# Kernel optimization log

Measured on AMD Instinct MI355X. Metric: run time of the kernel, lower is better.

The kernel has to match this reference:

```python
import jax, jax.numpy as jnp
import numpy as np
from jax import lax

N, T, K = 20000, 512, 12  # K = num_factors + 4


def setup_inputs() -> dict:
    key = jax.random.key(0)
    k1, k2, k3 = jax.random.split(key, 3)
    y = jax.random.normal(k1, (N, T), dtype=jnp.float32)
    f = jax.random.normal(k2, (T, K - 4), dtype=jnp.float32)
    # GARCH params must satisfy omega>0, a+b<1 for stationarity; scale uniforms
    theta = jax.random.uniform(k3, (N, T + 1, K), dtype=jnp.float32) * 0.4 + 0.01
    return {"y": y, "f": f, "theta": theta}


def reference(y, f, theta):
    th = theta[:, 1:, :]                      # [N, T, K]
    a = th[:, :, -3]                          # [N, T]
    b = th[:, :, -2]
    omega = th[:, :, -1]
    a_plus_b = a + b
    # epsilon = y - intercept - sum_f loadings * factors
    eps = y - th[:, :, 0] - jnp.einsum('ntf,tf->nt', th[:, :, 1:-3], f)
    eps2 = jnp.square(eps)
    # unconditional-variance init
    sigma2_0 = omega[:, 0] + a_plus_b[:, 0] * (
        jnp.mean(omega, axis=1) / (1.0 - jnp.mean(a_plus_b, axis=1)))
    # recurrence sigma2[t] = omega[t] + a[t]*sigma2[t-1] + b[t]*eps2[t-1]
    xs = (omega[:, 1:].T, a[:, 1:].T, b[:, 1:].T, eps2[:, :-1].T)  # time-major [T-1, N]

    def step(s, x):
        o_t, a_t, b_t, e_t = x
        s_new = o_t + a_t * s + b_t * e_t
        return s_new, s_new

    _, rest = lax.scan(step, sigma2_0, xs)    # rest: [T-1, N]
    sigma2 = jnp.concatenate([sigma2_0[:, None], rest.T], axis=1)  # [N, T]
    loss = jnp.mean(eps2 / sigma2 + jnp.log(sigma2))
    return (loss, eps, sigma2)
```

## Files before the change

### kernel.cpp

```cpp
#include <hip/hip_runtime.h>

#define N_ROWS 20000
#define T_DIM  512
#define K_DIM  12
#define TH_ROW ((T_DIM + 1) * K_DIM)
#define NBLK   (N_ROWS / 4)

__device__ __forceinline__ float fast_rcp(float x) { return __builtin_amdgcn_rcpf(x); }

__device__ __forceinline__ int tads(int tl) { return 9 * (tl >> 3) + (tl & 7); }

__device__ __forceinline__ void scan_chunk(
    const float* __restrict__ la, const float* __restrict__ lb,
    const float* __restrict__ lo, const float* __restrict__ le,
    int lane, int c, float s0, float& s_carry, float& e2_carry,
    float* __restrict__ sig_row, float& lsum)
{
    const int base = 9 * (lane >> 1) + 4 * (lane & 1);
    float av[4], bv[4], ov[4], e2v[4];
    #pragma unroll
    for (int i = 0; i < 4; ++i) {
        av[i] = la[base + i]; bv[i] = lb[base + i];
        ov[i] = lo[base + i]; e2v[i] = le[base + i];
    }
    float ep0 = e2_carry;
    if (lane > 0) ep0 = le[tads(4 * lane - 1)];

    float cv[4];
    cv[0] = fmaf(bv[0], ep0,    ov[0]);
    cv[1] = fmaf(bv[1], e2v[0], ov[1]);
    cv[2] = fmaf(bv[2], e2v[1], ov[2]);
    cv[3] = fmaf(bv[3], e2v[2], ov[3]);
    if (c == 0 && lane == 0) { av[0] = 0.f; cv[0] = s0; }

    float A = av[0], B = cv[0];
    #pragma unroll
    for (int i = 1; i < 4; ++i) { B = fmaf(av[i], B, cv[i]); A = av[i] * A; }

    float sA = A, sB = B;
    #pragma unroll
    for (int d = 1; d < 64; d <<= 1) {
        float Ap = __shfl_up(sA, d);
        float Bp = __shfl_up(sB, d);
        if (lane >= d) { sB = fmaf(sA, Bp, sB); sA = sA * Ap; }
    }
    float exA = __shfl_up(sA, 1), exB = __shfl_up(sB, 1);
    if (lane == 0) { exA = 1.f; exB = 0.f; }
    float s = fmaf(exA, s_carry, exB);

    #pragma unroll
    for (int i = 0; i < 4; ++i) {
        s = fmaf(av[i], s, cv[i]);
        sig_row[c * 256 + 4 * lane + i] = s;
        lsum += e2v[i] * fast_rcp(s) + __logf(s);
    }
    s_carry  = __shfl(s, 63);
    e2_carry = __shfl(e2v[3], 63);
}

__global__ __launch_bounds__(256) void garch_kernel(
    const float* __restrict__ y,
    const float* __restrict__ f,
    const float* __restrict__ theta,
    float* __restrict__ ws_part,
    float* __restrict__ out_eps,
    float* __restrict__ out_sig)
{
    __shared__ float lds_f[T_DIM * 9];
    __shared__ float lds_scan[4][4 * 288];
    __shared__ float lds_part[4];

    const int tid = threadIdx.x;
    for (int idx = tid; idx < T_DIM * 8; idx += 256) {
        int t = idx >> 3, j = idx & 7;
        lds_f[t * 9 + j] = f[idx];
    }
    __syncthreads();

    const int wave = tid >> 6;
    const int lane = tid & 63;
    const int n = blockIdx.x * 4 + wave;

    float* const wb = &lds_scan[wave][0];
    float* const la = wb;
    float* const lb = wb + 288;
    float* const lo = wb + 576;
    float* const le = wb + 864;

    const float* th_row = theta + (size_t)n * TH_ROW;
    const float* y_row  = y + (size_t)n * T_DIM;
    float* eps_row = out_eps + (size_t)n * T_DIM;
    float* sig_row = out_sig + (size_t)n * T_DIM;

    float a1[4], b1[4], o1[4], e1[4];
    float osum = 0.f, absum = 0.f;

    float4 pv0[4], pv1[4], pv2[4];
    float  py[4];
    #pragma unroll
    for (int i = 0; i < 4; ++i) {
        const int t = i * 64 + lane;
        const float4* p = (const float4*)(th_row + (size_t)(t + 1) * K_DIM);
        pv0[i] = p[0]; pv1[i] = p[1]; pv2[i] = p[2];
        py[i]  = y_row[t];
    }
    __builtin_amdgcn_sched_barrier(0);

    #pragma unroll
    for (int i = 0; i < 8; ++i) {
        const int slot = i & 3;
        const int t = i * 64 + lane;
        const float4 v0 = pv0[slot], v1 = pv1[slot], v2 = pv2[slot];
        const float  yv = py[slot];
        if (i < 4) {
            const int t2 = (i + 4) * 64 + lane;
            const float4* p = (const float4*)(th_row + (size_t)(t2 + 1) * K_DIM);
            pv0[slot] = p[0]; pv1[slot] = p[1]; pv2[slot] = p[2];
            py[slot]  = y_row[t2];
            __builtin_amdgcn_sched_barrier(0);
        }
        const float* fp = &lds_f[t * 9];
        float eps = yv - v0.x;
        eps = fmaf(-v0.y, fp[0], eps);
        eps = fmaf(-v0.z, fp[1], eps);
        eps = fmaf(-v0.w, fp[2], eps);
        eps = fmaf(-v1.x, fp[3], eps);
        eps = fmaf(-v1.y, fp[4], eps);
        eps = fmaf(-v1.z, fp[5], eps);
        eps = fmaf(-v1.w, fp[6], eps);
        eps = fmaf(-v2.x, fp[7], eps);
        eps_row[t] = eps;
        const float e2 = eps * eps;
        osum  += v2.w;
        absum += v2.y + v2.z;
        if (i < 4) {
            const int ad = tads(t);
            la[ad] = v2.y; lb[ad] = v2.z; lo[ad] = v2.w; le[ad] = e2;
        } else {
            a1[slot] = v2.y; b1[slot] = v2.z; o1[slot] = v2.w; e1[slot] = e2;
        }
    }

    #pragma unroll
    for (int d = 32; d; d >>= 1) {
        osum  += __shfl_xor(osum, d);
        absum += __shfl_xor(absum, d);
    }
    const float omean  = osum  * (1.0f / 512.0f);
    const float abmean = absum * (1.0f / 512.0f);
    const float s0 = lo[0] + (la[0] + lb[0]) * (omean / (1.0f - abmean));

    float s_carry = 0.f, e2_carry = 0.f, lsum = 0.f;
    scan_chunk(la, lb, lo, le, lane, 0, s0, s_carry, e2_carry, sig_row, lsum);

    #pragma unroll
    for (int i = 0; i < 4; ++i) {
        const int ad = tads(i * 64 + lane);
        la[ad] = a1[i]; lb[ad] = b1[i]; lo[ad] = o1[i]; le[ad] = e1[i];
    }
    scan_chunk(la, lb, lo, le, lane, 1, s0, s_carry, e2_carry, sig_row, lsum);

    #pragma unroll
    for (int d = 32; d; d >>= 1) lsum += __shfl_xor(lsum, d);
    if (lane == 0) lds_part[wave] = lsum;
    __syncthreads();
    if (tid == 0) {
        ws_part[blockIdx.x] = lds_part[0] + lds_part[1] + lds_part[2] + lds_part[3];
    }
}

__global__ __launch_bounds__(1024) void reduce_kernel(
    const float* __restrict__ ws_part, float* __restrict__ out_loss)
{
    __shared__ float w[16];
    float s = 0.f;
    for (int i = threadIdx.x; i < NBLK; i += 1024) s += ws_part[i];
    #pragma unroll
    for (int d = 32; d; d >>= 1) s += __shfl_xor(s, d);
    const int wave = threadIdx.x >> 6, lane = threadIdx.x & 63;
    if (lane == 0) w[wave] = s;
    __syncthreads();
    if (threadIdx.x == 0) {
        float t = 0.f;
        #pragma unroll
        for (int i = 0; i < 16; ++i) t += w[i];
        out_loss[0] = t * (1.0f / ((float)N_ROWS * (float)T_DIM));
    }
}

extern "C" void kernel_launch(void* const* d_in, const int* in_sizes, int n_in,
                              void* d_out, int out_size, void* d_ws, size_t ws_size,
                              hipStream_t stream) {
    const float* y     = (const float*)d_in[0];
    const float* f     = (const float*)d_in[1];
    const float* theta = (const float*)d_in[2];
    float* out = (float*)d_out;
    float* ws  = (float*)d_ws;

    float* out_eps = out + 1;
    float* out_sig = out + 1 + (size_t)N_ROWS * T_DIM;

    garch_kernel<<<NBLK, 256, 0, stream>>>(y, f, theta, ws, out_eps, out_sig);
    reduce_kernel<<<1, 1024, 0, stream>>>(ws, out);
}
```

Before: 125.7 us.

## Stage theta rows through LDS with async global_load_lds triple buffering

Replaces per-lane float4 register loads of theta, which were strided by 48 bytes and poorly coalesced, with contiguous 16-byte global_load_lds transfers into a per-wave triple-buffered LDS region, waited on with explicit vmcnt counters. The y row is preloaded entirely into registers and the eps stores are deferred until after the compute loop. This aims for fully coalesced theta reads and more loads in flight, at the cost of extra LDS (about 37KB more per block), which may lower occupancy, and reliance on hand-placed waitcnt correctness.

After: 130.2 us. +3.6%, slower.

```diff
diff --git a/kernel.cpp b/kernel.cpp
--- a/kernel.cpp
+++ b/kernel.cpp
@@ -9,6 +9,20 @@
 __device__ __forceinline__ float fast_rcp(float x) { return __builtin_amdgcn_rcpf(x); }
 
 __device__ __forceinline__ int tads(int tl) { return 9 * (tl >> 3) + (tl & 7); }
+
+__device__ __forceinline__ void gl_lds16(const float* g, float* l) {
+    __builtin_amdgcn_global_load_lds(
+        (const __attribute__((address_space(1))) void*)(g),
+        (__attribute__((address_space(3))) void*)(l),
+        16, 0, 0);
+}
+
+#define STAGE3(ii, dstbase) do {                                        \
+    const float* _s = th_row + 12 + (size_t)(ii) * 768 + lane * 4;      \
+    gl_lds16(_s,       (dstbase));                                      \
+    gl_lds16(_s + 256, (dstbase) + 256);                                \
+    gl_lds16(_s + 512, (dstbase) + 512);                                \
+} while (0)
 
 __device__ __forceinline__ void scan_chunk(
     const float* __restrict__ la, const float* __restrict__ lb,
@@ -66,8 +80,9 @@
     float* __restrict__ out_eps,
     float* __restrict__ out_sig)
 {
-    __shared__ float lds_f[T_DIM * 9];
-    __shared__ float lds_scan[4][4 * 288];
+    __shared__ __align__(16) float lds_f[T_DIM * 9];
+    __shared__ __align__(16) float lds_scan[4][4 * 288];
+    __shared__ __align__(16) float lds_th[4][3 * 768];
     __shared__ float lds_part[4];
 
     const int tid = threadIdx.x;
@@ -86,6 +101,7 @@
     float* const lb = wb + 288;
     float* const lo = wb + 576;
     float* const le = wb + 864;
+    float* const stw = &lds_th[wave][0];
 
     const float* th_row = theta + (size_t)n * TH_ROW;
     const float* y_row  = y + (size_t)n * T_DIM;
@@ -93,34 +109,33 @@
     float* sig_row = out_sig + (size_t)n * T_DIM;
 
     float a1[4], b1[4], o1[4], e1[4];
+    float epsv[8];
     float osum = 0.f, absum = 0.f;
 
-    float4 pv0[4], pv1[4], pv2[4];
-    float  py[4];
-    #pragma unroll
-    for (int i = 0; i < 4; ++i) {
+    float py[8];
+    #pragma unroll
+    for (int i = 0; i < 8; ++i) py[i] = y_row[i * 64 + lane];
+    __builtin_amdgcn_sched_barrier(0);
+    STAGE3(0, stw);
+    STAGE3(1, stw + 768);
+    __builtin_amdgcn_sched_barrier(0);
+
+    #pragma unroll
+    for (int i = 0; i < 8; ++i) {
+        if (i == 7) asm volatile("s_waitcnt vmcnt(0)" ::: "memory");
+        else        asm volatile("s_waitcnt vmcnt(3)" ::: "memory");
+
+        const float* buf = stw + (i % 3) * 768 + lane * 12;
+        const float4 v0 = *(const float4*)(buf);
+        const float4 v1 = *(const float4*)(buf + 4);
+        const float4 v2 = *(const float4*)(buf + 8);
+        __builtin_amdgcn_sched_barrier(0);
+        if (i < 6) STAGE3(i + 2, stw + ((i + 2) % 3) * 768);
+        __builtin_amdgcn_sched_barrier(0);
+
         const int t = i * 64 + lane;
-        const float4* p = (const float4*)(th_row + (size_t)(t + 1) * K_DIM);
-        pv0[i] = p[0]; pv1[i] = p[1]; pv2[i] = p[2];
-        py[i]  = y_row[t];
-    }
-    __builtin_amdgcn_sched_barrier(0);
-
-    #pragma unroll
-    for (int i = 0; i < 8; ++i) {
-        const int slot = i & 3;
-        const int t = i * 64 + lane;
-        const float4 v0 = pv0[slot], v1 = pv1[slot], v2 = pv2[slot];
-        const float  yv = py[slot];
-        if (i < 4) {
-            const int t2 = (i + 4) * 64 + lane;
-            const float4* p = (const float4*)(th_row + (size_t)(t2 + 1) * K_DIM);
-            pv0[slot] = p[0]; pv1[slot] = p[1]; pv2[slot] = p[2];
-            py[slot]  = y_row[t2];
-            __builtin_amdgcn_sched_barrier(0);
-        }
         const float* fp = &lds_f[t * 9];
-        float eps = yv - v0.x;
+        float eps = py[i] - v0.x;
         eps = fmaf(-v0.y, fp[0], eps);
         eps = fmaf(-v0.z, fp[1], eps);
         eps = fmaf(-v0.w, fp[2], eps);
@@ -129,7 +144,7 @@
         eps = fmaf(-v1.z, fp[5], eps);
         eps = fmaf(-v1.w, fp[6], eps);
         eps = fmaf(-v2.x, fp[7], eps);
-        eps_row[t] = eps;
+        epsv[i] = eps;
         const float e2 = eps * eps;
         osum  += v2.w;
         absum += v2.y + v2.z;
@@ -137,9 +152,12 @@
             const int ad = tads(t);
             la[ad] = v2.y; lb[ad] = v2.z; lo[ad] = v2.w; le[ad] = e2;
         } else {
-            a1[slot] = v2.y; b1[slot] = v2.z; o1[slot] = v2.w; e1[slot] = e2;
+            a1[i & 3] = v2.y; b1[i & 3] = v2.z; o1[i & 3] = v2.w; e1[i & 3] = e2;
         }
     }
+
+    #pragma unroll
+    for (int i = 0; i < 8; ++i) eps_row[i * 64 + lane] = epsv[i];
 
     #pragma unroll
     for (int d = 32; d; d >>= 1) {
```

## Process two rows per wave and prefetch next row's loads during scan

Applied to the files above, without the earlier changes.

Each wave now handles two rows instead of one, halving the block count, and adds occupancy hint 4 to launch_bounds. The second row's first theta/y loads are issued before the first row's scan runs, so global memory latency overlaps the shuffle-heavy scan. The f table load into shared memory is amortized over twice as many rows. The cost is more registers held live and fewer blocks in flight, which may reduce latency hiding from occupancy.

After: 137.9 us. 9.7% more time.

```diff
diff --git a/kernel.cpp b/kernel.cpp
--- a/kernel.cpp
+++ b/kernel.cpp
@@ -4,7 +4,8 @@
 #define T_DIM  512
 #define K_DIM  12
 #define TH_ROW ((T_DIM + 1) * K_DIM)
-#define NBLK   (N_ROWS / 4)
+#define RPB    8
+#define NBLK   (N_ROWS / RPB)
 
 __device__ __forceinline__ float fast_rcp(float x) { return __builtin_amdgcn_rcpf(x); }
 
@@ -58,45 +59,10 @@
     e2_carry = __shfl(e2v[3], 63);
 }
 
-__global__ __launch_bounds__(256) void garch_kernel(
-    const float* __restrict__ y,
-    const float* __restrict__ f,
-    const float* __restrict__ theta,
-    float* __restrict__ ws_part,
-    float* __restrict__ out_eps,
-    float* __restrict__ out_sig)
-{
-    __shared__ float lds_f[T_DIM * 9];
-    __shared__ float lds_scan[4][4 * 288];
-    __shared__ float lds_part[4];
-
-    const int tid = threadIdx.x;
-    for (int idx = tid; idx < T_DIM * 8; idx += 256) {
-        int t = idx >> 3, j = idx & 7;
-        lds_f[t * 9 + j] = f[idx];
-    }
-    __syncthreads();
-
-    const int wave = tid >> 6;
-    const int lane = tid & 63;
-    const int n = blockIdx.x * 4 + wave;
-
-    float* const wb = &lds_scan[wave][0];
-    float* const la = wb;
-    float* const lb = wb + 288;
-    float* const lo = wb + 576;
-    float* const le = wb + 864;
-
-    const float* th_row = theta + (size_t)n * TH_ROW;
-    const float* y_row  = y + (size_t)n * T_DIM;
-    float* eps_row = out_eps + (size_t)n * T_DIM;
-    float* sig_row = out_sig + (size_t)n * T_DIM;
-
-    float a1[4], b1[4], o1[4], e1[4];
-    float osum = 0.f, absum = 0.f;
-
-    float4 pv0[4], pv1[4], pv2[4];
-    float  py[4];
+__device__ __forceinline__ void prologue_loads(
+    const float* __restrict__ th_row, const float* __restrict__ y_row, int lane,
+    float4 (&pv0)[4], float4 (&pv1)[4], float4 (&pv2)[4], float (&py)[4])
+{
     #pragma unroll
     for (int i = 0; i < 4; ++i) {
         const int t = i * 64 + lane;
@@ -104,8 +70,17 @@
         pv0[i] = p[0]; pv1[i] = p[1]; pv2[i] = p[2];
         py[i]  = y_row[t];
     }
-    __builtin_amdgcn_sched_barrier(0);
-
+}
+
+__device__ __forceinline__ void phase1(
+    const float* __restrict__ th_row, const float* __restrict__ y_row, int lane,
+    float4 (&pv0)[4], float4 (&pv1)[4], float4 (&pv2)[4], float (&py)[4],
+    float* __restrict__ la, float* __restrict__ lb,
+    float* __restrict__ lo, float* __restrict__ le,
+    float* __restrict__ eps_row,
+    float (&a1)[4], float (&b1)[4], float (&o1)[4], float (&e1)[4],
+    float& osum, float& absum, const float* __restrict__ f)
+{
     #pragma unroll
     for (int i = 0; i < 8; ++i) {
         const int slot = i & 3;
@@ -119,7 +94,7 @@
             py[slot]  = y_row[t2];
             __builtin_amdgcn_sched_barrier(0);
         }
-        const float* fp = &lds_f[t * 9];
+        const float* fp = &f[t * 9];
         float eps = yv - v0.x;
         eps = fmaf(-v0.y, fp[0], eps);
         eps = fmaf(-v0.z, fp[1], eps);
@@ -140,25 +115,98 @@
             a1[slot] = v2.y; b1[slot] = v2.z; o1[slot] = v2.w; e1[slot] = e2;
         }
     }
+}
+
+__global__ __launch_bounds__(256, 4) void garch_kernel(
+    const float* __restrict__ y,
+    const float* __restrict__ f,
+    const float* __restrict__ theta,
+    float* __restrict__ ws_part,
+    float* __restrict__ out_eps,
+    float* __restrict__ out_sig)
+{
+    __shared__ float lds_f[T_DIM * 9];
+    __shared__ float lds_scan[4][4 * 288];
+    __shared__ float lds_part[4];
+
+    const int tid = threadIdx.x;
+    for (int idx = tid; idx < T_DIM * 8; idx += 256) {
+        int t = idx >> 3, j = idx & 7;
+        lds_f[t * 9 + j] = f[idx];
+    }
+    __syncthreads();
+
+    const int wave = tid >> 6;
+    const int lane = tid & 63;
+    const int n0 = blockIdx.x * RPB + wave * 2;
+
+    float* const wb = &lds_scan[wave][0];
+    float* const la = wb;
+    float* const lb = wb + 288;
+    float* const lo = wb + 576;
+    float* const le = wb + 864;
+
+    const float* th0 = theta + (size_t)n0 * TH_ROW;
+    const float* y0  = y + (size_t)n0 * T_DIM;
+    const float* th1 = th0 + TH_ROW;
+    const float* y1  = y0 + T_DIM;
+    float* eps0 = out_eps + (size_t)n0 * T_DIM;
+    float* sig0 = out_sig + (size_t)n0 * T_DIM;
+    float* eps1 = eps0 + T_DIM;
+    float* sig1 = sig0 + T_DIM;
+
+    float4 pv0[4], pv1[4], pv2[4];
+    float  py[4];
+    float a1[4], b1[4], o1[4], e1[4];
+    float lsum = 0.f;
+
+    prologue_loads(th0, y0, lane, pv0, pv1, pv2, py);
+    __builtin_amdgcn_sched_barrier(0);
+
+    float osum = 0.f, absum = 0.f;
+    phase1(th0, y0, lane, pv0, pv1, pv2, py, la, lb, lo, le, eps0,
+           a1, b1, o1, e1, osum, absum, lds_f);
 
     #pragma unroll
     for (int d = 32; d; d >>= 1) {
         osum  += __shfl_xor(osum, d);
         absum += __shfl_xor(absum, d);
     }
-    const float omean  = osum  * (1.0f / 512.0f);
-    const float abmean = absum * (1.0f / 512.0f);
-    const float s0 = lo[0] + (la[0] + lb[0]) * (omean / (1.0f - abmean));
-
-    float s_carry = 0.f, e2_carry = 0.f, lsum = 0.f;
-    scan_chunk(la, lb, lo, le, lane, 0, s0, s_carry, e2_carry, sig_row, lsum);
-
+    float s0 = lo[0] + (la[0] + lb[0]) *
+               ((osum * (1.0f / 512.0f)) / (1.0f - absum * (1.0f / 512.0f)));
+
+    prologue_loads(th1, y1, lane, pv0, pv1, pv2, py);
+    __builtin_amdgcn_sched_barrier(0);
+
+    float s_carry = 0.f, e2_carry = 0.f;
+    scan_chunk(la, lb, lo, le, lane, 0, s0, s_carry, e2_carry, sig0, lsum);
     #pragma unroll
     for (int i = 0; i < 4; ++i) {
         const int ad = tads(i * 64 + lane);
         la[ad] = a1[i]; lb[ad] = b1[i]; lo[ad] = o1[i]; le[ad] = e1[i];
     }
-    scan_chunk(la, lb, lo, le, lane, 1, s0, s_carry, e2_carry, sig_row, lsum);
+    scan_chunk(la, lb, lo, le, lane, 1, s0, s_carry, e2_carry, sig0, lsum);
+
+    osum = 0.f; absum = 0.f;
+    phase1(th1, y1, lane, pv0, pv1, pv2, py, la, lb, lo, le, eps1,
+           a1, b1, o1, e1, osum, absum, lds_f);
+
+    #pragma unroll
+    for (int d = 32; d; d >>= 1) {
+        osum  += __shfl_xor(osum, d);
+        absum += __shfl_xor(absum, d);
+    }
+    s0 = lo[0] + (la[0] + lb[0]) *
+         ((osum * (1.0f / 512.0f)) / (1.0f - absum * (1.0f / 512.0f)));
+
+    s_carry = 0.f; e2_carry = 0.f;
+    scan_chunk(la, lb, lo, le, lane, 0, s0, s_carry, e2_carry, sig1, lsum);
+    #pragma unroll
+    for (int i = 0; i < 4; ++i) {
+        const int ad = tads(i * 64 + lane);
+        la[ad] = a1[i]; lb[ad] = b1[i]; lo[ad] = o1[i]; le[ad] = e1[i];
+    }
+    scan_chunk(la, lb, lo, le, lane, 1, s0, s_carry, e2_carry, sig1, lsum);
 
     #pragma unroll
     for (int d = 32; d; d >>= 1) lsum += __shfl_xor(lsum, d);
```

## Use persistent grid with cross-row prefetch of next row during scan

Applied to the files above, without the earlier changes.

Replaces one-block-per-4-rows launch with a persistent grid of 1024 blocks where each wave loops over up to 5 rows. The next row's theta/y prologue loads are issued before the serial scan of the current row, overlapping global memory latency with the scan, and the f table is loaded into LDS once per block instead of per 4 rows. Occupancy hint of 4 blocks per CU is added; risk is tail imbalance (20000 rows over 4096 waves) and register pressure from the held prefetch.

Result: faster. 121.9 us (-3.0%).

```diff
diff --git a/kernel.cpp b/kernel.cpp
--- a/kernel.cpp
+++ b/kernel.cpp
@@ -4,7 +4,9 @@
 #define T_DIM  512
 #define K_DIM  12
 #define TH_ROW ((T_DIM + 1) * K_DIM)
-#define NBLK   (N_ROWS / 4)
+#define GRID_B 1024
+#define NWAVE  (GRID_B * 4)
+#define NPART  GRID_B
 
 __device__ __forceinline__ float fast_rcp(float x) { return __builtin_amdgcn_rcpf(x); }
 
@@ -58,45 +60,10 @@
     e2_carry = __shfl(e2v[3], 63);
 }
 
-__global__ __launch_bounds__(256) void garch_kernel(
-    const float* __restrict__ y,
-    const float* __restrict__ f,
-    const float* __restrict__ theta,
-    float* __restrict__ ws_part,
-    float* __restrict__ out_eps,
-    float* __restrict__ out_sig)
-{
-    __shared__ float lds_f[T_DIM * 9];
-    __shared__ float lds_scan[4][4 * 288];
-    __shared__ float lds_part[4];
-
-    const int tid = threadIdx.x;
-    for (int idx = tid; idx < T_DIM * 8; idx += 256) {
-        int t = idx >> 3, j = idx & 7;
-        lds_f[t * 9 + j] = f[idx];
-    }
-    __syncthreads();
-
-    const int wave = tid >> 6;
-    const int lane = tid & 63;
-    const int n = blockIdx.x * 4 + wave;
-
-    float* const wb = &lds_scan[wave][0];
-    float* const la = wb;
-    float* const lb = wb + 288;
-    float* const lo = wb + 576;
-    float* const le = wb + 864;
-
-    const float* th_row = theta + (size_t)n * TH_ROW;
-    const float* y_row  = y + (size_t)n * T_DIM;
-    float* eps_row = out_eps + (size_t)n * T_DIM;
-    float* sig_row = out_sig + (size_t)n * T_DIM;
-
-    float a1[4], b1[4], o1[4], e1[4];
-    float osum = 0.f, absum = 0.f;
-
-    float4 pv0[4], pv1[4], pv2[4];
-    float  py[4];
+__device__ __forceinline__ void prologue_loads(
+    const float* __restrict__ th_row, const float* __restrict__ y_row, int lane,
+    float4 (&pv0)[4], float4 (&pv1)[4], float4 (&pv2)[4], float (&py)[4])
+{
     #pragma unroll
     for (int i = 0; i < 4; ++i) {
         const int t = i * 64 + lane;
@@ -104,8 +71,17 @@
         pv0[i] = p[0]; pv1[i] = p[1]; pv2[i] = p[2];
         py[i]  = y_row[t];
     }
-    __builtin_amdgcn_sched_barrier(0);
-
+}
+
+__device__ __forceinline__ void phase1(
+    const float* __restrict__ th_row, const float* __restrict__ y_row, int lane,
+    float4 (&pv0)[4], float4 (&pv1)[4], float4 (&pv2)[4], float (&py)[4],
+    float* __restrict__ la, float* __restrict__ lb,
+    float* __restrict__ lo, float* __restrict__ le,
+    float* __restrict__ eps_row,
+    float (&a1)[4], float (&b1)[4], float (&o1)[4], float (&e1)[4],
+    float& osum, float& absum, const float* __restrict__ f)
+{
     #pragma unroll
     for (int i = 0; i < 8; ++i) {
         const int slot = i & 3;
@@ -119,7 +95,7 @@
             py[slot]  = y_row[t2];
             __builtin_amdgcn_sched_barrier(0);
         }
-        const float* fp = &lds_f[t * 9];
+        const float* fp = &f[t * 9];
         float eps = yv - v0.x;
         eps = fmaf(-v0.y, fp[0], eps);
         eps = fmaf(-v0.z, fp[1], eps);
@@ -140,25 +116,84 @@
             a1[slot] = v2.y; b1[slot] = v2.z; o1[slot] = v2.w; e1[slot] = e2;
         }
     }
-
-    #pragma unroll
-    for (int d = 32; d; d >>= 1) {
-        osum  += __shfl_xor(osum, d);
-        absum += __shfl_xor(absum, d);
-    }
-    const float omean  = osum  * (1.0f / 512.0f);
-    const float abmean = absum * (1.0f / 512.0f);
-    const float s0 = lo[0] + (la[0] + lb[0]) * (omean / (1.0f - abmean));
-
-    float s_carry = 0.f, e2_carry = 0.f, lsum = 0.f;
-    scan_chunk(la, lb, lo, le, lane, 0, s0, s_carry, e2_carry, sig_row, lsum);
-
-    #pragma unroll
-    for (int i = 0; i < 4; ++i) {
-        const int ad = tads(i * 64 + lane);
-        la[ad] = a1[i]; lb[ad] = b1[i]; lo[ad] = o1[i]; le[ad] = e1[i];
-    }
-    scan_chunk(la, lb, lo, le, lane, 1, s0, s_carry, e2_carry, sig_row, lsum);
+}
+
+__global__ __launch_bounds__(256, 4) void garch_kernel(
+    const float* __restrict__ y,
+    const float* __restrict__ f,
+    const float* __restrict__ theta,
+    float* __restrict__ ws_part,
+    float* __restrict__ out_eps,
+    float* __restrict__ out_sig)
+{
+    __shared__ float lds_f[T_DIM * 9];
+    __shared__ float lds_scan[4][4 * 288];
+    __shared__ float lds_part[4];
+
+    const int tid = threadIdx.x;
+    for (int idx = tid; idx < T_DIM * 8; idx += 256) {
+        int t = idx >> 3, j = idx & 7;
+        lds_f[t * 9 + j] = f[idx];
+    }
+    __syncthreads();
+
+    const int wave = tid >> 6;
+    const int lane = tid & 63;
+    const int wgid = blockIdx.x * 4 + wave;
+
+    float* const wb = &lds_scan[wave][0];
+    float* const la = wb;
+    float* const lb = wb + 288;
+    float* const lo = wb + 576;
+    float* const le = wb + 864;
+
+    float4 pv0[4], pv1[4], pv2[4];
+    float  py[4];
+    float a1[4], b1[4], o1[4], e1[4];
+    float lsum = 0.f;
+
+    prologue_loads(theta + (size_t)wgid * TH_ROW, y + (size_t)wgid * T_DIM,
+                   lane, pv0, pv1, pv2, py);
+    __builtin_amdgcn_sched_barrier(0);
+
+    #pragma unroll 1
+    for (int k = 0; k < 5; ++k) {
+        const int n = wgid + k * NWAVE;
+        if (n < N_ROWS) {
+            const float* th_row = theta + (size_t)n * TH_ROW;
+            const float* y_row  = y + (size_t)n * T_DIM;
+            float* eps_row = out_eps + (size_t)n * T_DIM;
+            float* sig_row = out_sig + (size_t)n * T_DIM;
+
+            float osum = 0.f, absum = 0.f;
+            phase1(th_row, y_row, lane, pv0, pv1, pv2, py,
+                   la, lb, lo, le, eps_row, a1, b1, o1, e1, osum, absum, lds_f);
+
+            #pragma unroll
+            for (int d = 32; d; d >>= 1) {
+                osum  += __shfl_xor(osum, d);
+                absum += __shfl_xor(absum, d);
+            }
+            const float s0 = lo[0] + (la[0] + lb[0]) *
+                ((osum * (1.0f / 512.0f)) / (1.0f - absum * (1.0f / 512.0f)));
+
+            const int n2 = n + NWAVE;
+            if (n2 < N_ROWS) {
+                prologue_loads(theta + (size_t)n2 * TH_ROW, y + (size_t)n2 * T_DIM,
+                               lane, pv0, pv1, pv2, py);
+                __builtin_amdgcn_sched_barrier(0);
+            }
+
+            float s_carry = 0.f, e2_carry = 0.f;
+            scan_chunk(la, lb, lo, le, lane, 0, s0, s_carry, e2_carry, sig_row, lsum);
+            #pragma unroll
+            for (int i = 0; i < 4; ++i) {
+                const int ad = tads(i * 64 + lane);
+                la[ad] = a1[i]; lb[ad] = b1[i]; lo[ad] = o1[i]; le[ad] = e1[i];
+            }
+            scan_chunk(la, lb, lo, le, lane, 1, s0, s_carry, e2_carry, sig_row, lsum);
+        }
+    }
 
     #pragma unroll
     for (int d = 32; d; d >>= 1) lsum += __shfl_xor(lsum, d);
@@ -174,7 +209,7 @@
 {
     __shared__ float w[16];
     float s = 0.f;
-    for (int i = threadIdx.x; i < NBLK; i += 1024) s += ws_part[i];
+    for (int i = threadIdx.x; i < NPART; i += 1024) s += ws_part[i];
     #pragma unroll
     for (int d = 32; d; d >>= 1) s += __shfl_xor(s, d);
     const int wave = threadIdx.x >> 6, lane = threadIdx.x & 63;
@@ -200,6 +235,6 @@
     float* out_eps = out + 1;
     float* out_sig = out + 1 + (size_t)N_ROWS * T_DIM;
 
-    garch_kernel<<<NBLK, 256, 0, stream>>>(y, f, theta, ws, out_eps, out_sig);
+    garch_kernel<<<GRID_B, 256, 0, stream>>>(y, f, theta, ws, out_eps, out_sig);
     reduce_kernel<<<1, 1024, 0, stream>>>(ws, out);
 }
```
